# Kernel optimization log

Hardware: AMD Instinct MI355X
Metric: run time of the kernel (lower is better)

Reference implementation:

```python
import jax, jax.numpy as jnp
import numpy as np

WS = 8          # window size (== stride, non-overlapping)
C_IN = 256
RED = 8
C_QK = C_IN // RED  # 32


def setup_inputs() -> dict:
    key = jax.random.key(0)
    ks = jax.random.split(key, 8)
    B, C, H, W = 4, C_IN, 256, 256
    x = jax.random.normal(ks[0], (B, C, H, W), dtype=jnp.float32)
    # 1x1 conv weights stored as [out_ch, in_ch] (kaiming-ish scale)
    wq = jax.random.normal(ks[1], (C_QK, C), dtype=jnp.float32) * np.sqrt(2.0 / C)
    wk = jax.random.normal(ks[2], (C_QK, C), dtype=jnp.float32) * np.sqrt(2.0 / C)
    wv = jax.random.normal(ks[3], (C, C), dtype=jnp.float32) * np.sqrt(2.0 / C)
    bq = jnp.zeros((C_QK,), dtype=jnp.float32)
    bk = jnp.zeros((C_QK,), dtype=jnp.float32)
    bv = jnp.zeros((C,), dtype=jnp.float32)
    gamma = jax.random.normal(ks[4], (1,), dtype=jnp.float32) * 0.5
    return {"x": x, "wq": wq, "bq": bq, "wk": wk, "bk": bk,
            "wv": wv, "bv": bv, "gamma": gamma}


def reference(x, wq, bq, wk, bk, wv, bv, gamma):
    B, C, H, W = x.shape
    Hw, Ww = H // WS, W // WS
    P = WS * WS  # 64 pixels per window
    # extract non-overlapping windows: [B,C,H,W] -> [N, C, P]
    xw = x.reshape(B, C, Hw, WS, Ww, WS)
    xw = xw.transpose(0, 2, 4, 1, 3, 5).reshape(B * Hw * Ww, C, P)
    # 1x1 conv projections (per-pixel channel GEMM)
    q = jnp.einsum('ncp,oc->nop', xw, wq) + bq[None, :, None]   # [N, Cqk, P]
    k = jnp.einsum('ncp,oc->nop', xw, wk) + bk[None, :, None]   # [N, Cqk, P]
    v = jnp.einsum('ncp,oc->nop', xw, wv) + bv[None, :, None]   # [N, C,   P]
    # attn[p, q_] = <Q[:,p], K[:,q_]> / sqrt(P), softmax over q_
    scale = 1.0 / np.sqrt(float(P))
    attn = jax.nn.softmax(jnp.einsum('ncp,ncq->npq', q, k) * scale, axis=-1)
    # out = V @ attn^T : out[c,p] = sum_q V[c,q] * attn[p,q]
    out = jnp.einsum('ncq,npq->ncp', v, attn)  # [N, C, P]
    # merge windows back: [N, C, P] -> [B, C, H, W]
    out = out.reshape(B, Hw, Ww, C, WS, WS)
    out = out.transpose(0, 3, 1, 4, 2, 5).reshape(B, C, H, W)
    return gamma * out + x
```

## Files before the change

kernel.cpp:

```cpp
#include <hip/hip_runtime.h>
#include <hip/hip_bf16.h>
#include <stdint.h>


#define CIN    256
#define WIMG   256
#define CH_STRIDE 65536

typedef __bf16 bf16x8 __attribute__((ext_vector_type(8)));
typedef float  f32x4  __attribute__((ext_vector_type(4)));

#define XT_OFF 0
#define QT_OFF 32768
#define KT_OFF 36864
#define PT_OFF 32768
#define HALF_LDS 40960

__device__ __forceinline__ int swz8(int p) { return (p ^ (p >> 3)) & 7; }

__device__ __forceinline__ uint32_t pack2(float lo, float hi) {
  union { __bf16 h[2]; uint32_t u; } un;
  un.h[0] = (__bf16)lo; un.h[1] = (__bf16)hi;
  return un.u;
}

union fragu { uint32_t u[4]; bf16x8 v; };

__global__ __launch_bounds__(256) void wprep_kernel(
    const float* __restrict__ wq, const float* __restrict__ wk,
    const float* __restrict__ wv, __bf16* __restrict__ out)
{
  int i = blockIdx.x * 256 + threadIdx.x;
  int off = i * 4;
  const float* src;
  if (off < 8192)       src = wq + off;
  else if (off < 16384) src = wk + (off - 8192);
  else                  src = wv + (off - 16384);
  float4 v = *(const float4*)src;
  __bf16 h[4] = {(__bf16)v.x, (__bf16)v.y, (__bf16)v.z, (__bf16)v.w};
  *(uint2*)(out + off) = *(const uint2*)h;
}

__global__ __launch_bounds__(512) void win_attn_kernel(
    const float* __restrict__ x,  const __bf16* __restrict__ wsb,
    const float* __restrict__ bq, const float* __restrict__ bk,
    const float* __restrict__ bv, const float* __restrict__ gamma,
    float* __restrict__ out, int nblk)
{
  extern __shared__ __attribute__((aligned(16))) unsigned char lds_raw[];

  int t = threadIdx.x;
  int half = t >> 8;
  int tt = t & 255;
  unsigned char* ldsb = lds_raw + half * HALF_LDS;

  int bid   = blockIdx.x;
  int chunk = nblk >> 3;
  int swz   = (bid & 7) * chunk + (bid >> 3);
  int b   = swz >> 9;
  int hw  = (swz >> 4) & 31;
  int wwp = swz & 15;
  int ww  = wwp * 2 + half;
  size_t win_off = (size_t)b * (CIN * CH_STRIDE) + (size_t)hw * 8 * WIMG + (size_t)ww * 8;
  const float* xw = x + win_off;
  float* ow = out + win_off;

  int w = tt >> 6, l = tt & 63, l16 = l & 15, lq = l >> 4;
  float g = gamma[0];

  int qkrow = (w & 1) * 16;
  bf16x8 wqkf[8];
  {
    const __bf16* qrow = wsb + ((w < 2) ? 0 : 8192) + (qkrow + l16) * 256 + lq * 8;
    #pragma unroll
    for (int ks = 0; ks < 8; ++ks) wqkf[ks] = *(const bf16x8*)(qrow + ks * 32);
  }

  #pragma unroll
  for (int it = 0; it < 8; ++it) {
    int id   = it * 256 + tt;
    int hf   = id & 1;
    int i    = (id >> 1) & 7;
    int c2   = id >> 4;
    const float* r0 = xw + (size_t)(2 * c2) * CH_STRIDE + i * WIMG + hf * 4;
    float4 va = *(const float4*)r0;
    float4 vb = *(const float4*)(r0 + CH_STRIDE);
    float ax[4] = {va.x, va.y, va.z, va.w};
    float bx[4] = {vb.x, vb.y, vb.z, vb.w};
    int blk = c2 >> 2;
    int sub = (c2 & 3) * 4;
    #pragma unroll
    for (int jj = 0; jj < 4; ++jj) {
      int p = i * 8 + hf * 4 + jj;
      *(uint32_t*)(ldsb + XT_OFF + p * 512 + ((blk ^ swz8(p)) << 4) + sub) =
          pack2(ax[jj], bx[jj]);
    }
  }
  __syncthreads();

  {
    f32x4 qacc[4] = {};
    #pragma unroll
    for (int ks = 0; ks < 8; ++ks) {
      bf16x8 xb[4];
      #pragma unroll
      for (int qi = 0; qi < 4; ++qi) {
        int p = qi * 16 + l16;
        xb[qi] = *(const bf16x8*)(ldsb + XT_OFF + p * 512 +
                                  (((ks * 4 + lq) ^ swz8(p)) << 4));
      }
      #pragma unroll
      for (int qi = 0; qi < 4; ++qi)
        qacc[qi] = __builtin_amdgcn_mfma_f32_16x16x32_bf16(wqkf[ks], xb[qi], qacc[qi], 0, 0, 0);
    }
    const float* bias = (w < 2) ? bq : bk;
    int lbase = (w < 2) ? QT_OFF : KT_OFF;
    #pragma unroll
    for (int r = 0; r < 4; ++r) {
      int c = qkrow + lq * 4 + r;
      float bb = bias[c];
      #pragma unroll
      for (int qi = 0; qi < 4; ++qi) {
        int p = qi * 16 + l16;
        *(__bf16*)(ldsb + lbase + p * 64 + (((c >> 3) ^ (p & 3)) << 4) + (c & 7) * 2) =
            (__bf16)(qacc[qi][r] + bb);
      }
    }
  }
  __syncthreads();

  uint32_t dP[4][2];
  {
    int pq = w * 16 + l16;
    bf16x8 qa = *(const bf16x8*)(ldsb + QT_OFF + pq * 64 + ((lq ^ (pq & 3)) << 4));
    f32x4 sacc[4];
    #pragma unroll
    for (int qi = 0; qi < 4; ++qi) {
      int pk = qi * 16 + l16;
      bf16x8 kb = *(const bf16x8*)(ldsb + KT_OFF + pk * 64 + ((lq ^ (pk & 3)) << 4));
      f32x4 z = {0.f, 0.f, 0.f, 0.f};
      sacc[qi] = __builtin_amdgcn_mfma_f32_16x16x32_bf16(kb, qa, z, 0, 0, 0);
    }
    float e[4][4];
    float mx = -1e30f;
    #pragma unroll
    for (int qi = 0; qi < 4; ++qi)
      #pragma unroll
      for (int r = 0; r < 4; ++r) {
        float v = sacc[qi][r] * 0.125f;
        e[qi][r] = v;
        mx = fmaxf(mx, v);
      }
    mx = fmaxf(mx, __shfl_xor(mx, 16));
    mx = fmaxf(mx, __shfl_xor(mx, 32));
    float s = 0.f;
    #pragma unroll
    for (int qi = 0; qi < 4; ++qi)
      #pragma unroll
      for (int r = 0; r < 4; ++r) {
        e[qi][r] = __expf(e[qi][r] - mx);
        s += e[qi][r];
      }
    s += __shfl_xor(s, 16);
    s += __shfl_xor(s, 32);
    float inv = 1.0f / s;
    #pragma unroll
    for (int qi = 0; qi < 4; ++qi) {
      dP[qi][0] = pack2(e[qi][0] * inv, e[qi][1] * inv);
      dP[qi][1] = pack2(e[qi][2] * inv, e[qi][3] * inv);
    }
  }

  uint32_t dV[4][4][2];
  {
    f32x4 vacc[4][4] = {};
    const __bf16* vrow = wsb + 16384 + (w * 64 + l16) * 256 + lq * 8;
    #pragma unroll
    for (int ks = 0; ks < 8; ++ks) {
      bf16x8 wvf[4];
      #pragma unroll
      for (int ci = 0; ci < 4; ++ci)
        wvf[ci] = *(const bf16x8*)(vrow + ci * 16 * 256 + ks * 32);
      bf16x8 xb[4];
      #pragma unroll
      for (int pi = 0; pi < 4; ++pi) {
        int p = pi * 16 + l16;
        xb[pi] = *(const bf16x8*)(ldsb + XT_OFF + p * 512 +
                                  (((ks * 4 + lq) ^ swz8(p)) << 4));
      }
      #pragma unroll
      for (int ci = 0; ci < 4; ++ci) {
        #pragma unroll
        for (int pi = 0; pi < 4; ++pi)
          vacc[pi][ci] = __builtin_amdgcn_mfma_f32_16x16x32_bf16(xb[pi], wvf[ci], vacc[pi][ci], 0, 0, 0);
      }
    }
    #pragma unroll
    for (int pi = 0; pi < 4; ++pi)
      #pragma unroll
      for (int ci = 0; ci < 4; ++ci) {
        dV[pi][ci][0] = pack2(vacc[pi][ci][0], vacc[pi][ci][1]);
        dV[pi][ci][1] = pack2(vacc[pi][ci][2], vacc[pi][ci][3]);
      }
  }
  __syncthreads();

  {
    int q = w * 16 + l16;
    int qm = q & 7;
    #pragma unroll
    for (int qi = 0; qi < 4; ++qi) {
      int blk = (((qi >> 1) * 4) + lq) ^ qm;
      uint2 val; val.x = dP[qi][0]; val.y = dP[qi][1];
      *(uint2*)(ldsb + PT_OFF + q * 128 + blk * 16 + (qi & 1) * 8) = val;
    }
  }
  __syncthreads();

  f32x4 oacc[4][4] = {};
  #pragma unroll
  for (int ks = 0; ks < 2; ++ks) {
    bf16x8 Pf[4];
    #pragma unroll
    for (int bj = 0; bj < 4; ++bj) {
      int q = bj * 16 + l16;
      int blk = (ks * 4 + lq) ^ (q & 7);
      Pf[bj] = *(const bf16x8*)(ldsb + PT_OFF + q * 128 + blk * 16);
    }
    #pragma unroll
    for (int ci = 0; ci < 4; ++ci) {
      fragu Vf;
      Vf.u[0] = dV[2 * ks][ci][0];
      Vf.u[1] = dV[2 * ks][ci][1];
      Vf.u[2] = dV[2 * ks + 1][ci][0];
      Vf.u[3] = dV[2 * ks + 1][ci][1];
      #pragma unroll
      for (int bj = 0; bj < 4; ++bj)
        oacc[ci][bj] = __builtin_amdgcn_mfma_f32_16x16x32_bf16(Pf[bj], Vf.v, oacc[ci][bj], 0, 0, 0);
    }
  }

  #pragma unroll
  for (int ci = 0; ci < 4; ++ci) {
    int c = w * 64 + ci * 16 + l16;
    size_t cbase = (size_t)c * CH_STRIDE;
    float bvc = bv[c];
    int chi = c >> 3, clo = (c & 7) * 2;
    #pragma unroll
    for (int bj = 0; bj < 4; ++bj) {
      int p0 = bj * 16 + lq * 4;
      float xr[4];
      #pragma unroll
      for (int r = 0; r < 4; ++r) {
        int p = p0 + r;
        xr[r] = (float)(*(const __bf16*)(ldsb + XT_OFF + p * 512 +
                                         ((chi ^ swz8(p)) << 4) + clo));
      }
      float4 o;
      o.x = g * (oacc[ci][bj][0] + bvc) + xr[0];
      o.y = g * (oacc[ci][bj][1] + bvc) + xr[1];
      o.z = g * (oacc[ci][bj][2] + bvc) + xr[2];
      o.w = g * (oacc[ci][bj][3] + bvc) + xr[3];
      *(float4*)(ow + cbase + (size_t)(p0 >> 3) * WIMG + (p0 & 7)) = o;
    }
  }
}

extern "C" void kernel_launch(void* const* d_in, const int* in_sizes, int n_in,
                              void* d_out, int out_size, void* d_ws, size_t ws_size,
                              hipStream_t stream) {
  const float* x     = (const float*)d_in[0];
  const float* wq    = (const float*)d_in[1];
  const float* bq    = (const float*)d_in[2];
  const float* wk    = (const float*)d_in[3];
  const float* bk    = (const float*)d_in[4];
  const float* wv    = (const float*)d_in[5];
  const float* bv    = (const float*)d_in[6];
  const float* gamma = (const float*)d_in[7];
  float* out = (float*)d_out;
  __bf16* wsb = (__bf16*)d_ws;

  hipFuncSetAttribute((const void*)win_attn_kernel,
                      hipFuncAttributeMaxDynamicSharedMemorySize, 2 * HALF_LDS);

  wprep_kernel<<<dim3(80), dim3(256), 0, stream>>>(wq, wk, wv, wsb);

  int B = in_sizes[0] / (CIN * CH_STRIDE);
  int nblk = B * 512;
  win_attn_kernel<<<dim3(nblk), dim3(512), 2 * HALF_LDS, stream>>>(
      x, wsb, bq, bk, bv, gamma, out, nblk);
}
```

Before: 255.4 us.

## Compute Q/K projections in registers per wave and halve P LDS buffer

Each wave now computes its own Q tile and the full K projection directly into MFMA fragment registers. This removes the LDS round trip for Q/K and one barrier, at the cost of redundant K computation across the four waves (about double the QK MFMA work). The P matrix is staged through LDS in two halves with a smaller padded buffer, which lowers LDS per block and may raise occupancy but adds a barrier pair.

```diff
diff --git a/kernel.cpp b/kernel.cpp
--- a/kernel.cpp
+++ b/kernel.cpp
@@ -11,10 +11,8 @@
 typedef float  f32x4  __attribute__((ext_vector_type(4)));
 
 #define XT_OFF 0
-#define QT_OFF 32768
-#define KT_OFF 36864
 #define PT_OFF 32768
-#define HALF_LDS 40960
+#define HALF_LDS 37888
 
 __device__ __forceinline__ int swz8(int p) { return (p ^ (p >> 3)) & 7; }
 
@@ -68,14 +66,6 @@
   int w = tt >> 6, l = tt & 63, l16 = l & 15, lq = l >> 4;
   float g = gamma[0];
 
-  int qkrow = (w & 1) * 16;
-  bf16x8 wqkf[8];
-  {
-    const __bf16* qrow = wsb + ((w < 2) ? 0 : 8192) + (qkrow + l16) * 256 + lq * 8;
-    #pragma unroll
-    for (int ks = 0; ks < 8; ++ks) wqkf[ks] = *(const bf16x8*)(qrow + ks * 32);
-  }
-
   #pragma unroll
   for (int it = 0; it < 8; ++it) {
     int id   = it * 256 + tt;
@@ -98,8 +88,12 @@
   }
   __syncthreads();
 
-  {
-    f32x4 qacc[4] = {};
+  fragu kf[4], qf;
+  {
+    f32x4 kacc[4][2] = {};
+    f32x4 qacc[2] = {};
+    const __bf16* wqrow = wsb + l16 * 256 + lq * 8;
+    const __bf16* wkrow = wsb + 8192 + l16 * 256 + lq * 8;
     #pragma unroll
     for (int ks = 0; ks < 8; ++ks) {
       bf16x8 xb[4];
@@ -110,36 +104,39 @@
                                   (((ks * 4 + lq) ^ swz8(p)) << 4));
       }
       #pragma unroll
-      for (int qi = 0; qi < 4; ++qi)
-        qacc[qi] = __builtin_amdgcn_mfma_f32_16x16x32_bf16(wqkf[ks], xb[qi], qacc[qi], 0, 0, 0);
-    }
-    const float* bias = (w < 2) ? bq : bk;
-    int lbase = (w < 2) ? QT_OFF : KT_OFF;
-    #pragma unroll
-    for (int r = 0; r < 4; ++r) {
-      int c = qkrow + lq * 4 + r;
-      float bb = bias[c];
-      #pragma unroll
-      for (int qi = 0; qi < 4; ++qi) {
-        int p = qi * 16 + l16;
-        *(__bf16*)(ldsb + lbase + p * 64 + (((c >> 3) ^ (p & 3)) << 4) + (c & 7) * 2) =
-            (__bf16)(qacc[qi][r] + bb);
-      }
-    }
-  }
-  __syncthreads();
+      for (int j = 0; j < 2; ++j) {
+        bf16x8 wkf = *(const bf16x8*)(wkrow + j * 16 * 256 + ks * 32);
+        bf16x8 wqf = *(const bf16x8*)(wqrow + j * 16 * 256 + ks * 32);
+        qacc[j] = __builtin_amdgcn_mfma_f32_16x16x32_bf16(wqf, xb[w], qacc[j], 0, 0, 0);
+        #pragma unroll
+        for (int qi = 0; qi < 4; ++qi)
+          kacc[qi][j] = __builtin_amdgcn_mfma_f32_16x16x32_bf16(wkf, xb[qi], kacc[qi][j], 0, 0, 0);
+      }
+    }
+    float4 bq0 = *(const float4*)(bq + lq * 4);
+    float4 bq1 = *(const float4*)(bq + 16 + lq * 4);
+    float4 bk0 = *(const float4*)(bk + lq * 4);
+    float4 bk1 = *(const float4*)(bk + 16 + lq * 4);
+    qf.u[0] = pack2(qacc[0][0] + bq0.x, qacc[0][1] + bq0.y);
+    qf.u[1] = pack2(qacc[0][2] + bq0.z, qacc[0][3] + bq0.w);
+    qf.u[2] = pack2(qacc[1][0] + bq1.x, qacc[1][1] + bq1.y);
+    qf.u[3] = pack2(qacc[1][2] + bq1.z, qacc[1][3] + bq1.w);
+    #pragma unroll
+    for (int qi = 0; qi < 4; ++qi) {
+      kf[qi].u[0] = pack2(kacc[qi][0][0] + bk0.x, kacc[qi][0][1] + bk0.y);
+      kf[qi].u[1] = pack2(kacc[qi][0][2] + bk0.z, kacc[qi][0][3] + bk0.w);
+      kf[qi].u[2] = pack2(kacc[qi][1][0] + bk1.x, kacc[qi][1][1] + bk1.y);
+      kf[qi].u[3] = pack2(kacc[qi][1][2] + bk1.z, kacc[qi][1][3] + bk1.w);
+    }
+  }
 
   uint32_t dP[4][2];
   {
-    int pq = w * 16 + l16;
-    bf16x8 qa = *(const bf16x8*)(ldsb + QT_OFF + pq * 64 + ((lq ^ (pq & 3)) << 4));
     f32x4 sacc[4];
     #pragma unroll
     for (int qi = 0; qi < 4; ++qi) {
-      int pk = qi * 16 + l16;
-      bf16x8 kb = *(const bf16x8*)(ldsb + KT_OFF + pk * 64 + ((lq ^ (pk & 3)) << 4));
       f32x4 z = {0.f, 0.f, 0.f, 0.f};
-      sacc[qi] = __builtin_amdgcn_mfma_f32_16x16x32_bf16(kb, qa, z, 0, 0, 0);
+      sacc[qi] = __builtin_amdgcn_mfma_f32_16x16x32_bf16(kf[qi].v, qf.v, z, 0, 0, 0);
     }
     float e[4][4];
     float mx = -1e30f;
@@ -171,6 +168,12 @@
     }
   }
 
+  {
+    int q = w * 16 + l16;
+    uint4 p0; p0.x = dP[0][0]; p0.y = dP[0][1]; p0.z = dP[1][0]; p0.w = dP[1][1];
+    *(uint4*)(ldsb + PT_OFF + q * 80 + lq * 16) = p0;
+  }
+
   uint32_t dV[4][4][2];
   {
     f32x4 vacc[4][4] = {};
@@ -205,35 +208,41 @@
   }
   __syncthreads();
 
-  {
-    int q = w * 16 + l16;
-    int qm = q & 7;
-    #pragma unroll
-    for (int qi = 0; qi < 4; ++qi) {
-      int blk = (((qi >> 1) * 4) + lq) ^ qm;
-      uint2 val; val.x = dP[qi][0]; val.y = dP[qi][1];
-      *(uint2*)(ldsb + PT_OFF + q * 128 + blk * 16 + (qi & 1) * 8) = val;
-    }
-  }
-  __syncthreads();
-
   f32x4 oacc[4][4] = {};
-  #pragma unroll
-  for (int ks = 0; ks < 2; ++ks) {
+  {
     bf16x8 Pf[4];
     #pragma unroll
-    for (int bj = 0; bj < 4; ++bj) {
-      int q = bj * 16 + l16;
-      int blk = (ks * 4 + lq) ^ (q & 7);
-      Pf[bj] = *(const bf16x8*)(ldsb + PT_OFF + q * 128 + blk * 16);
-    }
+    for (int bj = 0; bj < 4; ++bj)
+      Pf[bj] = *(const bf16x8*)(ldsb + PT_OFF + (bj * 16 + l16) * 80 + lq * 16);
     #pragma unroll
     for (int ci = 0; ci < 4; ++ci) {
       fragu Vf;
-      Vf.u[0] = dV[2 * ks][ci][0];
-      Vf.u[1] = dV[2 * ks][ci][1];
-      Vf.u[2] = dV[2 * ks + 1][ci][0];
-      Vf.u[3] = dV[2 * ks + 1][ci][1];
+      Vf.u[0] = dV[0][ci][0]; Vf.u[1] = dV[0][ci][1];
+      Vf.u[2] = dV[1][ci][0]; Vf.u[3] = dV[1][ci][1];
+      #pragma unroll
+      for (int bj = 0; bj < 4; ++bj)
+        oacc[ci][bj] = __builtin_amdgcn_mfma_f32_16x16x32_bf16(Pf[bj], Vf.v, oacc[ci][bj], 0, 0, 0);
+    }
+  }
+  __syncthreads();
+
+  {
+    int q = w * 16 + l16;
+    uint4 p1; p1.x = dP[2][0]; p1.y = dP[2][1]; p1.z = dP[3][0]; p1.w = dP[3][1];
+    *(uint4*)(ldsb + PT_OFF + q * 80 + lq * 16) = p1;
+  }
+  __syncthreads();
+
+  {
+    bf16x8 Pf[4];
+    #pragma unroll
+    for (int bj = 0; bj < 4; ++bj)
+      Pf[bj] = *(const bf16x8*)(ldsb + PT_OFF + (bj * 16 + l16) * 80 + lq * 16);
+    #pragma unroll
+    for (int ci = 0; ci < 4; ++ci) {
+      fragu Vf;
+      Vf.u[0] = dV[2][ci][0]; Vf.u[1] = dV[2][ci][1];
+      Vf.u[2] = dV[3][ci][0]; Vf.u[3] = dV[3][ci][1];
       #pragma unroll
       for (int bj = 0; bj < 4; ++bj)
         oacc[ci][bj] = __builtin_amdgcn_mfma_f32_16x16x32_bf16(Pf[bj], Vf.v, oacc[ci][bj], 0, 0, 0);
```

Result: slower. 408.9 us (+60.1%).

## Stage input channels in two halves to shrink LDS and fuse QK/V projections

Applied to the files above, without the earlier changes.

The window's x tile is now loaded into LDS in two 128-channel chunks instead of all 256 at once, halving the per-window X buffer and cutting the total LDS footprint per block. The Q/K and V projection MFMAs are fused into one loop over each chunk, so every LDS fragment of x is read once for both. The residual for the first 128 channels is re-read from global memory as fp32, since those channels are no longer resident in LDS. This trades an extra sync, some global re-reads and more live accumulator registers for lower LDS use, which may allow more blocks per CU.

```diff
diff --git a/kernel.cpp b/kernel.cpp
--- a/kernel.cpp
+++ b/kernel.cpp
@@ -11,10 +11,10 @@
 typedef float  f32x4  __attribute__((ext_vector_type(4)));
 
 #define XT_OFF 0
-#define QT_OFF 32768
-#define KT_OFF 36864
-#define PT_OFF 32768
-#define HALF_LDS 40960
+#define QT_OFF 16384
+#define KT_OFF 20480
+#define PT_OFF 16384
+#define HALF_LDS 24576
 
 __device__ __forceinline__ int swz8(int p) { return (p ^ (p >> 3)) & 7; }
 
@@ -55,8 +55,8 @@
   unsigned char* ldsb = lds_raw + half * HALF_LDS;
 
   int bid   = blockIdx.x;
-  int chunk = nblk >> 3;
-  int swz   = (bid & 7) * chunk + (bid >> 3);
+  int chunkb = nblk >> 3;
+  int swz   = (bid & 7) * chunkb + (bid >> 3);
   int b   = swz >> 9;
   int hw  = (swz >> 4) & 31;
   int wwp = swz & 15;
@@ -69,50 +69,63 @@
   float g = gamma[0];
 
   int qkrow = (w & 1) * 16;
-  bf16x8 wqkf[8];
-  {
-    const __bf16* qrow = wsb + ((w < 2) ? 0 : 8192) + (qkrow + l16) * 256 + lq * 8;
-    #pragma unroll
-    for (int ks = 0; ks < 8; ++ks) wqkf[ks] = *(const bf16x8*)(qrow + ks * 32);
-  }
-
-  #pragma unroll
-  for (int it = 0; it < 8; ++it) {
-    int id   = it * 256 + tt;
-    int hf   = id & 1;
-    int i    = (id >> 1) & 7;
-    int c2   = id >> 4;
-    const float* r0 = xw + (size_t)(2 * c2) * CH_STRIDE + i * WIMG + hf * 4;
-    float4 va = *(const float4*)r0;
-    float4 vb = *(const float4*)(r0 + CH_STRIDE);
-    float ax[4] = {va.x, va.y, va.z, va.w};
-    float bx[4] = {vb.x, vb.y, vb.z, vb.w};
-    int blk = c2 >> 2;
-    int sub = (c2 & 3) * 4;
-    #pragma unroll
-    for (int jj = 0; jj < 4; ++jj) {
-      int p = i * 8 + hf * 4 + jj;
-      *(uint32_t*)(ldsb + XT_OFF + p * 512 + ((blk ^ swz8(p)) << 4) + sub) =
-          pack2(ax[jj], bx[jj]);
-    }
-  }
-  __syncthreads();
-
-  {
-    f32x4 qacc[4] = {};
-    #pragma unroll
-    for (int ks = 0; ks < 8; ++ks) {
+  f32x4 qacc[4]    = {};
+  f32x4 vacc[4][4] = {};
+  const __bf16* wqkrow = wsb + ((w < 2) ? 0 : 8192) + (qkrow + l16) * 256 + lq * 8;
+  const __bf16* vrow   = wsb + 16384 + (w * 64 + l16) * 256 + lq * 8;
+
+  #pragma unroll
+  for (int ck = 0; ck < 2; ++ck) {
+    #pragma unroll
+    for (int it = 0; it < 4; ++it) {
+      int id   = it * 256 + tt;
+      int hf   = id & 1;
+      int i    = (id >> 1) & 7;
+      int c2   = id >> 4;
+      const float* r0 = xw + (size_t)(ck * 128 + 2 * c2) * CH_STRIDE + i * WIMG + hf * 4;
+      float4 va = *(const float4*)r0;
+      float4 vb = *(const float4*)(r0 + CH_STRIDE);
+      float ax[4] = {va.x, va.y, va.z, va.w};
+      float bx[4] = {vb.x, vb.y, vb.z, vb.w};
+      int blk = c2 >> 2;
+      int sub = (c2 & 3) * 4;
+      #pragma unroll
+      for (int jj = 0; jj < 4; ++jj) {
+        int p = i * 8 + hf * 4 + jj;
+        *(uint32_t*)(ldsb + XT_OFF + p * 256 + ((blk ^ swz8(p)) << 4) + sub) =
+            pack2(ax[jj], bx[jj]);
+      }
+    }
+    __syncthreads();
+
+    #pragma unroll
+    for (int ks = 0; ks < 4; ++ks) {
+      bf16x8 wvf[4];
+      #pragma unroll
+      for (int ci = 0; ci < 4; ++ci)
+        wvf[ci] = *(const bf16x8*)(vrow + ci * 16 * 256 + ck * 128 + ks * 32);
+      bf16x8 wqkf = *(const bf16x8*)(wqkrow + ck * 128 + ks * 32);
       bf16x8 xb[4];
       #pragma unroll
       for (int qi = 0; qi < 4; ++qi) {
         int p = qi * 16 + l16;
-        xb[qi] = *(const bf16x8*)(ldsb + XT_OFF + p * 512 +
+        xb[qi] = *(const bf16x8*)(ldsb + XT_OFF + p * 256 +
                                   (((ks * 4 + lq) ^ swz8(p)) << 4));
       }
       #pragma unroll
       for (int qi = 0; qi < 4; ++qi)
-        qacc[qi] = __builtin_amdgcn_mfma_f32_16x16x32_bf16(wqkf[ks], xb[qi], qacc[qi], 0, 0, 0);
-    }
+        qacc[qi] = __builtin_amdgcn_mfma_f32_16x16x32_bf16(wqkf, xb[qi], qacc[qi], 0, 0, 0);
+      #pragma unroll
+      for (int ci = 0; ci < 4; ++ci) {
+        #pragma unroll
+        for (int pi = 0; pi < 4; ++pi)
+          vacc[pi][ci] = __builtin_amdgcn_mfma_f32_16x16x32_bf16(xb[pi], wvf[ci], vacc[pi][ci], 0, 0, 0);
+      }
+    }
+    if (ck == 0) __syncthreads();
+  }
+
+  {
     const float* bias = (w < 2) ? bq : bk;
     int lbase = (w < 2) ? QT_OFF : KT_OFF;
     #pragma unroll
@@ -172,37 +185,13 @@
   }
 
   uint32_t dV[4][4][2];
-  {
-    f32x4 vacc[4][4] = {};
-    const __bf16* vrow = wsb + 16384 + (w * 64 + l16) * 256 + lq * 8;
-    #pragma unroll
-    for (int ks = 0; ks < 8; ++ks) {
-      bf16x8 wvf[4];
-      #pragma unroll
-      for (int ci = 0; ci < 4; ++ci)
-        wvf[ci] = *(const bf16x8*)(vrow + ci * 16 * 256 + ks * 32);
-      bf16x8 xb[4];
-      #pragma unroll
-      for (int pi = 0; pi < 4; ++pi) {
-        int p = pi * 16 + l16;
-        xb[pi] = *(const bf16x8*)(ldsb + XT_OFF + p * 512 +
-                                  (((ks * 4 + lq) ^ swz8(p)) << 4));
-      }
-      #pragma unroll
-      for (int ci = 0; ci < 4; ++ci) {
-        #pragma unroll
-        for (int pi = 0; pi < 4; ++pi)
-          vacc[pi][ci] = __builtin_amdgcn_mfma_f32_16x16x32_bf16(xb[pi], wvf[ci], vacc[pi][ci], 0, 0, 0);
-      }
-    }
-    #pragma unroll
-    for (int pi = 0; pi < 4; ++pi)
-      #pragma unroll
-      for (int ci = 0; ci < 4; ++ci) {
-        dV[pi][ci][0] = pack2(vacc[pi][ci][0], vacc[pi][ci][1]);
-        dV[pi][ci][1] = pack2(vacc[pi][ci][2], vacc[pi][ci][3]);
-      }
-  }
+  #pragma unroll
+  for (int pi = 0; pi < 4; ++pi)
+    #pragma unroll
+    for (int ci = 0; ci < 4; ++ci) {
+      dV[pi][ci][0] = pack2(vacc[pi][ci][0], vacc[pi][ci][1]);
+      dV[pi][ci][1] = pack2(vacc[pi][ci][2], vacc[pi][ci][3]);
+    }
   __syncthreads();
 
   {
@@ -245,23 +234,31 @@
     int c = w * 64 + ci * 16 + l16;
     size_t cbase = (size_t)c * CH_STRIDE;
     float bvc = bv[c];
-    int chi = c >> 3, clo = (c & 7) * 2;
     #pragma unroll
     for (int bj = 0; bj < 4; ++bj) {
       int p0 = bj * 16 + lq * 4;
+      size_t off = cbase + (size_t)(p0 >> 3) * WIMG + (p0 & 7);
       float xr[4];
-      #pragma unroll
-      for (int r = 0; r < 4; ++r) {
-        int p = p0 + r;
-        xr[r] = (float)(*(const __bf16*)(ldsb + XT_OFF + p * 512 +
-                                         ((chi ^ swz8(p)) << 4) + clo));
+      if (w >= 2) {
+        int cc = c - 128;
+        int blk = cc >> 3;
+        int sub = ((cc >> 1) & 3) * 4 + (cc & 1) * 2;
+        #pragma unroll
+        for (int r = 0; r < 4; ++r) {
+          int p = p0 + r;
+          xr[r] = (float)(*(const __bf16*)(ldsb + XT_OFF + p * 256 +
+                                           ((blk ^ swz8(p)) << 4) + sub));
+        }
+      } else {
+        float4 xv = *(const float4*)(xw + off);
+        xr[0] = xv.x; xr[1] = xv.y; xr[2] = xv.z; xr[3] = xv.w;
       }
       float4 o;
       o.x = g * (oacc[ci][bj][0] + bvc) + xr[0];
       o.y = g * (oacc[ci][bj][1] + bvc) + xr[1];
       o.z = g * (oacc[ci][bj][2] + bvc) + xr[2];
       o.w = g * (oacc[ci][bj][3] + bvc) + xr[3];
-      *(float4*)(ow + cbase + (size_t)(p0 >> 3) * WIMG + (p0 & 7)) = o;
+      *(float4*)(ow + off) = o;
     }
   }
 }
```

Result: faster. 246.0 us (-3.7%).
